# Kernel tuning notes

Hardware: AMD Instinct MI355X
Metric: run time of the kernel (lower is better)

## Reference

```python
import jax, jax.numpy as jnp
import numpy as np

L, V, Tctx, D, H, DFF = 4, 32000, 1024, 1024, 16, 4096
HD = D // H
B, T = 2, 1024


def _ln(x, w, b):
    mu = jnp.mean(x, axis=-1, keepdims=True)
    var = jnp.var(x, axis=-1, keepdims=True)
    return (x - mu) * jax.lax.rsqrt(var + 1e-5) * w + b


def setup_inputs() -> dict:
    key = jax.random.key(0)
    ks = jax.random.split(key, 8)
    s = 0.02
    return {
        "idx": jax.random.randint(ks[0], (B, T), 0, V),
        "wte": jax.random.normal(ks[1], (V, D), jnp.float32) * s,
        "wpe": jax.random.normal(ks[2], (Tctx, D), jnp.float32) * s,
        "ln1_w": jnp.ones((L, D), jnp.float32),
        "ln1_b": jnp.zeros((L, D), jnp.float32),
        "qkv_w": jax.random.normal(ks[3], (L, 3 * D, D), jnp.float32) * s,
        "qkv_b": jnp.zeros((L, 3 * D), jnp.float32),
        "proj_w": jax.random.normal(ks[4], (L, D, D), jnp.float32) * s,
        "proj_b": jnp.zeros((L, D), jnp.float32),
        "ln2_w": jnp.ones((L, D), jnp.float32),
        "ln2_b": jnp.zeros((L, D), jnp.float32),
        "fc1_w": jax.random.normal(ks[5], (L, DFF, D), jnp.float32) * s,
        "fc1_b": jnp.zeros((L, DFF), jnp.float32),
        "fc2_w": jax.random.normal(ks[6], (L, D, DFF), jnp.float32) * s,
        "fc2_b": jnp.zeros((L, D), jnp.float32),
        "lnf_w": jnp.ones((D,), jnp.float32),
        "lnf_b": jnp.zeros((D,), jnp.float32),
    }


def reference(idx, wte, wpe, ln1_w, ln1_b, qkv_w, qkv_b, proj_w, proj_b,
              ln2_w, ln2_b, fc1_w, fc1_b, fc2_w, fc2_b, lnf_w, lnf_b):
    b, t = idx.shape
    x = wte[idx] + wpe[:t]  # (B,T,D); dropout=0 (eval)
    scale = 1.0 / jnp.sqrt(jnp.float32(HD))
    causal = jnp.tril(jnp.ones((t, t), bool))  # (T,T)

    def block(x, p):
        (l1w, l1b, qw, qb, pw, pb, l2w, l2b, f1w, f1b, f2w, f2b) = p
        h = _ln(x, l1w, l1b)
        qkv = h @ qw.T + qb  # (B,T,3D)
        q, k, v = jnp.split(qkv, 3, axis=-1)
        q = q.reshape(b, t, H, HD)
        k = k.reshape(b, t, H, HD)
        v = v.reshape(b, t, H, HD)
        att = jnp.einsum('bqhd,bkhd->bhqk', q, k) * scale
        att = jnp.where(causal, att, -jnp.inf)
        att = jax.nn.softmax(att, axis=-1)
        y = jnp.einsum('bhqk,bkhd->bqhd', att, v).reshape(b, t, D)
        x = x + y @ pw.T + pb
        h2 = _ln(x, l2w, l2b)
        h2 = jax.nn.gelu(h2 @ f1w.T + f1b, approximate=False)
        x = x + h2 @ f2w.T + f2b
        return x, None

    params = (ln1_w, ln1_b, qkv_w, qkv_b, proj_w, proj_b,
              ln2_w, ln2_b, fc1_w, fc1_b, fc2_w, fc2_b)
    x, _ = jax.lax.scan(block, x, params)
    x = _ln(x, lnf_w, lnf_b)
    logits = x @ wte.T  # weight-tied lm_head
    return logits
```

## Files before the change

### kernel.cpp

```cpp
#include <hip/hip_runtime.h>
#include <hip/hip_bf16.h>
#include <cstdint>
#include <cstddef>

using hb = __hip_bfloat16;
typedef __bf16 bf16x8 __attribute__((ext_vector_type(8)));
typedef float f32x4 __attribute__((ext_vector_type(4)));
typedef const __attribute__((address_space(1))) void* gptr_t;
typedef __attribute__((address_space(3))) void* lptr_t;

namespace {
constexpr int L_ = 4, V_ = 32000, D_ = 1024, H_ = 16, DFF_ = 4096, HD_ = 64;
constexpr int B_ = 2, T_ = 1024;
constexpr int BT = B_ * T_;
constexpr int PSTR = 56;
constexpr int MTILES = BT / 128;
}

__global__ __launch_bounds__(256) void k_cast_bf16(const float* __restrict__ in,
                                                   hb* __restrict__ out, int n4) {
  int i = blockIdx.x * 256 + threadIdx.x;
  const int stride = gridDim.x * 256;
  for (; i < n4; i += stride) {
    float4 v = reinterpret_cast<const float4*>(in)[i];
    union { hb h[4]; ushort4 u; } t;
    t.h[0] = __float2bfloat16(v.x);
    t.h[1] = __float2bfloat16(v.y);
    t.h[2] = __float2bfloat16(v.z);
    t.h[3] = __float2bfloat16(v.w);
    reinterpret_cast<ushort4*>(out)[i] = t.u;
  }
}

__global__ __launch_bounds__(256) void k_embed(const int* __restrict__ idx,
                                               const float* __restrict__ wte,
                                               const float* __restrict__ wpe,
                                               float* __restrict__ x) {
  const int i = blockIdx.x * 256 + threadIdx.x;
  const int row = i >> 10;
  const int d = i & 1023;
  const int t = row & (T_ - 1);
  const int tok = idx[row];
  x[i] = wte[(size_t)tok * D_ + d] + wpe[(size_t)t * D_ + d];
}

__global__ __launch_bounds__(256) void k_ln(const float* __restrict__ x,
                                            const float* __restrict__ w,
                                            const float* __restrict__ b,
                                            hb* __restrict__ out) {
  const int row = blockIdx.x;
  const int tid = threadIdx.x;
  const float4 v = reinterpret_cast<const float4*>(x + (size_t)row * D_)[tid];
  float s = v.x + v.y + v.z + v.w;
  float ss = v.x * v.x + v.y * v.y + v.z * v.z + v.w * v.w;
#pragma unroll
  for (int o = 32; o; o >>= 1) { s += __shfl_xor(s, o); ss += __shfl_xor(ss, o); }
  __shared__ float rs[4], rss[4];
  const int wid = tid >> 6;
  if ((tid & 63) == 0) { rs[wid] = s; rss[wid] = ss; }
  __syncthreads();
  s = rs[0] + rs[1] + rs[2] + rs[3];
  ss = rss[0] + rss[1] + rss[2] + rss[3];
  const float mu = s * (1.f / D_);
  const float var = ss * (1.f / D_) - mu * mu;
  const float rstd = rsqrtf(var + 1e-5f);
  const float4 wv = reinterpret_cast<const float4*>(w)[tid];
  const float4 bv = reinterpret_cast<const float4*>(b)[tid];
  union { hb h[4]; ushort4 u; } t;
  t.h[0] = __float2bfloat16((v.x - mu) * rstd * wv.x + bv.x);
  t.h[1] = __float2bfloat16((v.y - mu) * rstd * wv.y + bv.y);
  t.h[2] = __float2bfloat16((v.z - mu) * rstd * wv.z + bv.z);
  t.h[3] = __float2bfloat16((v.w - mu) * rstd * wv.w + bv.w);
  reinterpret_cast<ushort4*>(out + (size_t)row * D_)[tid] = t.u;
}

__global__ __launch_bounds__(256) void k_vtrans(const hb* __restrict__ qkv,
                                                hb* __restrict__ vt) {
  __shared__ __align__(16) hb tile[64][66];
  const int bh = blockIdx.x;
  const int b = bh >> 4, h = bh & (H_ - 1);
  const int t0 = blockIdx.y * 64;
  const int tid = threadIdx.x;
  const int tl = tid >> 2, dc = (tid & 3) * 16;
  const hb* src = qkv + ((size_t)(b * T_ + t0 + tl) * 3 * D_) + 2 * D_ + h * HD_ + dc;
  *reinterpret_cast<bf16x8*>(&tile[tl][dc]) = *reinterpret_cast<const bf16x8*>(src);
  *reinterpret_cast<bf16x8*>(&tile[tl][dc + 8]) = *reinterpret_cast<const bf16x8*>(src + 8);
  __syncthreads();
  const int d = tid & 63, tj = tid >> 6;
  hb o[16];
#pragma unroll
  for (int j = 0; j < 16; ++j) o[j] = tile[tj * 16 + j][d];
  bf16x8* dst = reinterpret_cast<bf16x8*>(vt + ((size_t)bh * HD_ + d) * T_ + t0 + tj * 16);
  dst[0] = *reinterpret_cast<bf16x8*>(&o[0]);
  dst[1] = *reinterpret_cast<bf16x8*>(&o[8]);
}

__global__ __launch_bounds__(256) void k_attn(const hb* __restrict__ qkv,
                                              const hb* __restrict__ vt,
                                              hb* __restrict__ y) {
  const int lane = threadIdx.x & 63;
  const int wid = threadIdx.x >> 6;
  const int gw = blockIdx.x * 4 + wid;
  const int qt = 63 - (gw & 63);
  const int bh = gw >> 6;
  const int h = bh & (H_ - 1), b = bh >> 4;
  const int q0 = qt * 16;
  const int lr = lane & 15, g = lane >> 4;

  __shared__ __align__(16) hb plds[4][16 * PSTR];
  hb* pw = plds[wid];

  const size_t qrow = ((size_t)(b * T_ + q0 + lr) * 3 * D_) + (size_t)h * HD_;
  const bf16x8 qa0 = *reinterpret_cast<const bf16x8*>(qkv + qrow + g * 8);
  const bf16x8 qa1 = *reinterpret_cast<const bf16x8*>(qkv + qrow + 32 + g * 8);

  const f32x4 z = {0.f, 0.f, 0.f, 0.f};
  float m[4] = {-1e30f, -1e30f, -1e30f, -1e30f};
  float lsum[4] = {0.f, 0.f, 0.f, 0.f};
  f32x4 o[4];
#pragma unroll
  for (int i = 0; i < 4; ++i) o[i] = z;

  const int nkv = (q0 + 47) >> 5;
  for (int kt = 0; kt < nkv; ++kt) {
    const int kv0 = kt * 32;
    f32x4 s[2];
#pragma unroll
    for (int nt = 0; nt < 2; ++nt) {
      const size_t krow =
          ((size_t)(b * T_ + kv0 + nt * 16 + lr) * 3 * D_) + D_ + (size_t)h * HD_;
      const bf16x8 kb0 = *reinterpret_cast<const bf16x8*>(qkv + krow + g * 8);
      const bf16x8 kb1 = *reinterpret_cast<const bf16x8*>(qkv + krow + 32 + g * 8);
      f32x4 acc = z;
      acc = __builtin_amdgcn_mfma_f32_16x16x32_bf16(qa0, kb0, acc, 0, 0, 0);
      acc = __builtin_amdgcn_mfma_f32_16x16x32_bf16(qa1, kb1, acc, 0, 0, 0);
      s[nt] = acc;
    }
#pragma unroll
    for (int r = 0; r < 4; ++r) {
      const int qg = q0 + g * 4 + r;
      const float s0 = (kv0 + lr <= qg) ? s[0][r] * 0.125f : -1e30f;
      const float s1 = (kv0 + 16 + lr <= qg) ? s[1][r] * 0.125f : -1e30f;
      float rmax = fmaxf(s0, s1);
#pragma unroll
      for (int off = 1; off < 16; off <<= 1) rmax = fmaxf(rmax, __shfl_xor(rmax, off));
      const float mn = fmaxf(m[r], rmax);
      const float c = __expf(m[r] - mn);
      m[r] = mn;
      const float p0 = __expf(s0 - mn);
      const float p1 = __expf(s1 - mn);
      float ps = p0 + p1;
#pragma unroll
      for (int off = 1; off < 16; off <<= 1) ps += __shfl_xor(ps, off);
      lsum[r] = lsum[r] * c + ps;
#pragma unroll
      for (int dt = 0; dt < 4; ++dt) o[dt][r] *= c;
      pw[(g * 4 + r) * PSTR + lr] = __float2bfloat16(p0);
      pw[(g * 4 + r) * PSTR + 16 + lr] = __float2bfloat16(p1);
    }
    const bf16x8 pa = *reinterpret_cast<const bf16x8*>(&pw[lr * PSTR + g * 8]);
#pragma unroll
    for (int dt = 0; dt < 4; ++dt) {
      const bf16x8 vb = *reinterpret_cast<const bf16x8*>(
          vt + ((size_t)bh * HD_ + dt * 16 + lr) * T_ + kv0 + g * 8);
      o[dt] = __builtin_amdgcn_mfma_f32_16x16x32_bf16(pa, vb, o[dt], 0, 0, 0);
    }
  }
#pragma unroll
  for (int dt = 0; dt < 4; ++dt) {
#pragma unroll
    for (int r = 0; r < 4; ++r) {
      const size_t oo =
          ((size_t)(b * T_ + q0 + g * 4 + r) * D_) + h * HD_ + dt * 16 + lr;
      y[oo] = __float2bfloat16(o[dt][r] / lsum[r]);
    }
  }
}

template <int EPI, bool OBF, int BN>
__global__ __launch_bounds__(256) void gemm_bt(const hb* __restrict__ A,
                                               const hb* __restrict__ Bw,
                                               const float* __restrict__ bias,
                                               const float* resid,
                                               void* outv, int M, int N, int K) {
  constexpr int WMR = (BN == 128) ? 4 : 2;
  __shared__ __align__(16) hb As[2][128 * 32];
  __shared__ __align__(16) hb Bs[2][BN * 32];
  const int tid = threadIdx.x, lane = tid & 63, wid = tid >> 6;

  const int nwg = gridDim.x;
  const int d = blockIdx.x;
  const int wg = (d & 7) * (nwg >> 3) + (d >> 3);
  const int m0 = (wg & (MTILES - 1)) * 128;
  const int n0 = (wg / MTILES) * BN;

  const int wr = (BN == 128) ? (wid >> 1) : wid;
  const int wc = (BN == 128) ? (wid & 1) : 0;

  f32x4 acc[WMR][4];
  const f32x4 z = {0.f, 0.f, 0.f, 0.f};
#pragma unroll
  for (int i = 0; i < WMR; ++i)
#pragma unroll
    for (int j = 0; j < 4; ++j) acc[i][j] = z;

  const int e0 = tid * 8;
  auto stage = [&](int buf, int k0) {
#pragma unroll
    for (int r = 0; r < 2; ++r) {
      const int e = e0 + r * 2048;
      const int row = e >> 5, col = e & 31;
      __builtin_amdgcn_global_load_lds(
          (gptr_t)(A + (size_t)(m0 + row) * K + k0 + col), (lptr_t)(&As[buf][e]), 16, 0, 0);
    }
#pragma unroll
    for (int r = 0; r < BN / 64; ++r) {
      const int e = e0 + r * 2048;
      const int row = e >> 5, col = e & 31;
      __builtin_amdgcn_global_load_lds(
          (gptr_t)(Bw + (size_t)(n0 + row) * K + k0 + col), (lptr_t)(&Bs[buf][e]), 16, 0, 0);
    }
  };

  stage(0, 0);
  stage(1, 32);

  const int nt = K >> 5;
  const int lr = lane & 15, lk = (lane >> 4) * 8;
  for (int t = 0; t < nt; ++t) {
    const int cur = t & 1;
    if (t + 1 < nt) {
      if constexpr (BN == 128)
        asm volatile("s_waitcnt vmcnt(4)" ::: "memory");
      else
        asm volatile("s_waitcnt vmcnt(3)" ::: "memory");
    } else {
      asm volatile("s_waitcnt vmcnt(0)" ::: "memory");
    }
    asm volatile("s_barrier" ::: "memory");

    bf16x8 af[WMR], bfr[4];
#pragma unroll
    for (int i = 0; i < WMR; ++i)
      af[i] = *reinterpret_cast<const bf16x8*>(
          &As[cur][(wr * (WMR * 16) + i * 16 + lr) * 32 + lk]);
#pragma unroll
    for (int j = 0; j < 4; ++j)
      bfr[j] = *reinterpret_cast<const bf16x8*>(
          &Bs[cur][(wc * 64 + j * 16 + lr) * 32 + lk]);
#pragma unroll
    for (int i = 0; i < WMR; ++i)
#pragma unroll
      for (int j = 0; j < 4; ++j)
        acc[i][j] = __builtin_amdgcn_mfma_f32_16x16x32_bf16(af[i], bfr[j], acc[i][j], 0, 0, 0);

    asm volatile("s_waitcnt lgkmcnt(0)" ::: "memory");
    asm volatile("s_barrier" ::: "memory");
    if (t + 2 < nt) stage(cur, (t + 2) * 32);
  }

  const int lc = lane & 15, lr4 = (lane >> 4) * 4;
#pragma unroll
  for (int i = 0; i < WMR; ++i) {
    const int grow0 = m0 + wr * (WMR * 16) + i * 16 + lr4;
#pragma unroll
    for (int j = 0; j < 4; ++j) {
      const int gcol = n0 + wc * 64 + j * 16 + lc;
      const float bv = bias ? bias[gcol] : 0.f;
#pragma unroll
      for (int r = 0; r < 4; ++r) {
        const size_t oo = (size_t)(grow0 + r) * N + gcol;
        float val = acc[i][j][r] + bv;
        if constexpr (EPI == 1) val += resid[oo];
        if constexpr (EPI == 2) val = 0.5f * val * (1.f + erff(val * 0.70710678118f));
        if constexpr (OBF)
          reinterpret_cast<hb*>(outv)[oo] = __float2bfloat16(val);
        else
          reinterpret_cast<float*>(outv)[oo] = val;
      }
    }
  }
}

#define MM16(ABASE, AF, BF)                                                     \
  _Pragma("unroll") for (int i_ = 0; i_ < 4; ++i_)                              \
      _Pragma("unroll") for (int j_ = 0; j_ < 4; ++j_)                          \
          acc[(ABASE) + i_][j_] = __builtin_amdgcn_mfma_f32_16x16x32_bf16(      \
              (AF)[i_], (BF)[j_], acc[(ABASE) + i_][j_], 0, 0, 0);

__global__ __launch_bounds__(512, 2) void gemm_lmhead(const hb* __restrict__ A,
                                                      const hb* __restrict__ Bw,
                                                      float* __restrict__ out) {
  constexpr int K = 1024, N = 32000, NT = K / 32;
  __shared__ __align__(16) hb As[4][256][32];
  __shared__ __align__(16) hb Bs[4][256][32];
  const int tid = threadIdx.x, lane = tid & 63, wid = tid >> 6;
  const int nwg = gridDim.x;
  const int dd = blockIdx.x;
  const int wg = (dd & 7) * (nwg >> 3) + (dd >> 3);
  const int m0 = (wg & 7) * 256;
  const int n0 = (wg >> 3) * 256;
  const int wr = wid >> 2, wc = wid & 3;
  const int lr = lane & 15;
  const int rc8 = (((lane >> 4) ^ ((lr >> 1) & 3)) & 3) * 8;

  f32x4 acc[8][4];
  const f32x4 z = {0.f, 0.f, 0.f, 0.f};
#pragma unroll
  for (int i = 0; i < 8; ++i)
#pragma unroll
    for (int j = 0; j < 4; ++j) acc[i][j] = z;

  const int rr = tid >> 2;
  const int cs = tid & 3;
  const int cc = cs ^ ((tid >> 3) & 3);

  auto stageA = [&](int b, int t) {
#pragma unroll
    for (int q = 0; q < 2; ++q) {
      const int row = q * 128 + rr;
      __builtin_amdgcn_global_load_lds(
          (gptr_t)(A + (size_t)(m0 + row) * K + t * 32 + cc * 8),
          (lptr_t)(&As[b][row][cs * 8]), 16, 0, 0);
    }
  };
  auto stageB = [&](int b, int t) {
#pragma unroll
    for (int q = 0; q < 2; ++q) {
      const int row = q * 128 + rr;
      __builtin_amdgcn_global_load_lds(
          (gptr_t)(Bw + (size_t)(n0 + row) * K + t * 32 + cc * 8),
          (lptr_t)(&Bs[b][row][cs * 8]), 16, 0, 0);
    }
  };
  auto dsA = [&](int b, int mh, bf16x8* af) {
#pragma unroll
    for (int i = 0; i < 4; ++i)
      af[i] = *reinterpret_cast<const bf16x8*>(
          &As[b][wr * 128 + mh * 64 + i * 16 + lr][rc8]);
  };
  auto dsB = [&](int b, bf16x8* bf) {
#pragma unroll
    for (int j = 0; j < 4; ++j)
      bf[j] = *reinterpret_cast<const bf16x8*>(&Bs[b][wc * 64 + j * 16 + lr][rc8]);
  };

  auto tile = [&](int t, bool stg, int vm) {
    const int c = t & 3;
    const int b3 = (t + 3) & 3;
    bf16x8 af[4], bf[4];
    dsA(c, 0, af);
    dsB(c, bf);
    if (stg) stageA(b3, t + 3);
    __builtin_amdgcn_s_barrier();
    asm volatile("s_waitcnt lgkmcnt(0)" ::: "memory");
    __builtin_amdgcn_s_setprio(1);
    MM16(0, af, bf)
    __builtin_amdgcn_s_setprio(0);
    __builtin_amdgcn_s_barrier();
    dsA(c, 1, af);
    if (stg) stageB(b3, t + 3);
    if (vm == 8)
      asm volatile("s_waitcnt vmcnt(8)" ::: "memory");
    else if (vm == 4)
      asm volatile("s_waitcnt vmcnt(4)" ::: "memory");
    else if (vm == 0)
      asm volatile("s_waitcnt vmcnt(0)" ::: "memory");
    __builtin_amdgcn_s_barrier();
    asm volatile("s_waitcnt lgkmcnt(0)" ::: "memory");
    __builtin_amdgcn_s_setprio(1);
    MM16(4, af, bf)
    __builtin_amdgcn_s_setprio(0);
    __builtin_amdgcn_s_barrier();
  };

  stageA(0, 0); stageB(0, 0);
  stageA(1, 1); stageB(1, 1);
  stageA(2, 2); stageB(2, 2);
  asm volatile("s_waitcnt vmcnt(8)" ::: "memory");
  __builtin_amdgcn_s_barrier();

  for (int t = 0; t < NT - 3; ++t) tile(t, true, 8);
  tile(NT - 3, false, 4);
  tile(NT - 2, false, 0);
  tile(NT - 1, false, -1);

  const int lc = lane & 15, lr4 = (lane >> 4) * 4;
#pragma unroll
  for (int i2 = 0; i2 < 8; ++i2) {
    const int grow0 = m0 + wr * 128 + i2 * 16 + lr4;
#pragma unroll
    for (int j = 0; j < 4; ++j) {
      const int gcol = n0 + wc * 64 + j * 16 + lc;
#pragma unroll
      for (int r = 0; r < 4; ++r)
        out[(size_t)(grow0 + r) * N + gcol] = acc[i2][j][r];
    }
  }
}

extern "C" void kernel_launch(void* const* d_in, const int* in_sizes, int n_in,
                              void* d_out, int out_size, void* d_ws, size_t ws_size,
                              hipStream_t stream) {
  const int* idx = (const int*)d_in[0];
  const float* wte = (const float*)d_in[1];
  const float* wpe = (const float*)d_in[2];
  const float* ln1_w = (const float*)d_in[3];
  const float* ln1_b = (const float*)d_in[4];
  const float* qkv_w = (const float*)d_in[5];
  const float* qkv_b = (const float*)d_in[6];
  const float* proj_w = (const float*)d_in[7];
  const float* proj_b = (const float*)d_in[8];
  const float* ln2_w = (const float*)d_in[9];
  const float* ln2_b = (const float*)d_in[10];
  const float* fc1_w = (const float*)d_in[11];
  const float* fc1_b = (const float*)d_in[12];
  const float* fc2_w = (const float*)d_in[13];
  const float* fc2_b = (const float*)d_in[14];
  const float* lnf_w = (const float*)d_in[15];
  const float* lnf_b = (const float*)d_in[16];

  char* ws = (char*)d_ws;
  size_t off = 0;
  auto alloc = [&](size_t bytes) -> void* {
    void* p = ws + off;
    off += (bytes + 255) & ~(size_t)255;
    return p;
  };
  hb* wte_bf = (hb*)alloc((size_t)V_ * D_ * 2);
  hb* qkvw_bf = (hb*)alloc((size_t)L_ * 3 * D_ * D_ * 2);
  hb* projw_bf = (hb*)alloc((size_t)L_ * D_ * D_ * 2);
  hb* fc1w_bf = (hb*)alloc((size_t)L_ * DFF_ * D_ * 2);
  hb* fc2w_bf = (hb*)alloc((size_t)L_ * D_ * DFF_ * 2);
  float* x = (float*)alloc((size_t)BT * D_ * 4);
  hb* hbuf = (hb*)alloc((size_t)BT * D_ * 2);
  hb* qkvbuf = (hb*)alloc((size_t)BT * 3 * D_ * 2);
  hb* ybuf = (hb*)alloc((size_t)BT * D_ * 2);
  hb* gbuf = (hb*)alloc((size_t)BT * DFF_ * 2);
  hb* vtbuf = (hb*)alloc((size_t)B_ * H_ * HD_ * T_ * 2);

  auto cast = [&](const float* src, hb* dst, size_t n) {
    int n4 = (int)(n / 4);
    int blocks = (n4 + 255) / 256;
    if (blocks > 4096) blocks = 4096;
    k_cast_bf16<<<blocks, 256, 0, stream>>>(src, dst, n4);
  };
  cast(wte, wte_bf, (size_t)V_ * D_);
  cast(qkv_w, qkvw_bf, (size_t)L_ * 3 * D_ * D_);
  cast(proj_w, projw_bf, (size_t)L_ * D_ * D_);
  cast(fc1_w, fc1w_bf, (size_t)L_ * DFF_ * D_);
  cast(fc2_w, fc2w_bf, (size_t)L_ * D_ * DFF_);

  k_embed<<<BT * D_ / 256, 256, 0, stream>>>(idx, wte, wpe, x);

  for (int l = 0; l < L_; ++l) {
    k_ln<<<BT, 256, 0, stream>>>(x, ln1_w + l * D_, ln1_b + l * D_, hbuf);
    gemm_bt<0, true, 128><<<MTILES * (3 * D_ / 128), 256, 0, stream>>>(
        hbuf, qkvw_bf + (size_t)l * 3 * D_ * D_, qkv_b + (size_t)l * 3 * D_, nullptr,
        qkvbuf, BT, 3 * D_, D_);
    k_vtrans<<<dim3(B_ * H_, T_ / 64), 256, 0, stream>>>(qkvbuf, vtbuf);
    k_attn<<<(B_ * H_ * (T_ / 16)) / 4, 256, 0, stream>>>(qkvbuf, vtbuf, ybuf);
    gemm_bt<1, false, 64><<<MTILES * (D_ / 64), 256, 0, stream>>>(
        ybuf, projw_bf + (size_t)l * D_ * D_, proj_b + (size_t)l * D_, x, x, BT, D_, D_);
    k_ln<<<BT, 256, 0, stream>>>(x, ln2_w + l * D_, ln2_b + l * D_, hbuf);
    gemm_bt<2, true, 128><<<MTILES * (DFF_ / 128), 256, 0, stream>>>(
        hbuf, fc1w_bf + (size_t)l * DFF_ * D_, fc1_b + (size_t)l * DFF_, nullptr,
        gbuf, BT, DFF_, D_);
    gemm_bt<1, false, 64><<<MTILES * (D_ / 64), 256, 0, stream>>>(
        gbuf, fc2w_bf + (size_t)l * D_ * DFF_, fc2_b + (size_t)l * D_, x, x, BT, D_, DFF_);
  }

  k_ln<<<BT, 256, 0, stream>>>(x, lnf_w, lnf_b, hbuf);
  gemm_lmhead<<<8 * (V_ / 256), 512, 0, stream>>>(hbuf, wte_bf, (float*)d_out);
}
```

Before: 1.214 ms.

## Fuse V-transpose into QKV GEMM epilogue, merge casts and embed+LN

The QKV GEMM epilogue now also writes the V part straight into the transposed per-head layout, so the separate transpose kernel is gone. The five weight-cast launches become one multi-range kernel. Embedding is fused with the first layer's LayerNorm, which saves one launch and one pass over x. The cost is extra scattered 8-byte stores in the QKV epilogue.

```diff
diff --git a/kernel.cpp b/kernel.cpp
--- a/kernel.cpp
+++ b/kernel.cpp
@@ -17,11 +17,10 @@
 constexpr int MTILES = BT / 128;
 }
 
-__global__ __launch_bounds__(256) void k_cast_bf16(const float* __restrict__ in,
-                                                   hb* __restrict__ out, int n4) {
-  int i = blockIdx.x * 256 + threadIdx.x;
-  const int stride = gridDim.x * 256;
-  for (; i < n4; i += stride) {
+__device__ __forceinline__ void cast_range(const float* __restrict__ in,
+                                           hb* __restrict__ out, int n4,
+                                           int base, int stride) {
+  for (int i = base; i < n4; i += stride) {
     float4 v = reinterpret_cast<const float4*>(in)[i];
     union { hb h[4]; ushort4 u; } t;
     t.h[0] = __float2bfloat16(v.x);
@@ -32,16 +31,55 @@
   }
 }
 
-__global__ __launch_bounds__(256) void k_embed(const int* __restrict__ idx,
-                                               const float* __restrict__ wte,
-                                               const float* __restrict__ wpe,
-                                               float* __restrict__ x) {
-  const int i = blockIdx.x * 256 + threadIdx.x;
-  const int row = i >> 10;
-  const int d = i & 1023;
+__global__ __launch_bounds__(256) void k_cast5(
+    const float* s0, hb* d0, int n0, const float* s1, hb* d1, int n1,
+    const float* s2, hb* d2, int n2, const float* s3, hb* d3, int n3,
+    const float* s4, hb* d4, int n4) {
+  const int base = blockIdx.x * 256 + threadIdx.x;
+  const int stride = gridDim.x * 256;
+  cast_range(s0, d0, n0, base, stride);
+  cast_range(s1, d1, n1, base, stride);
+  cast_range(s2, d2, n2, base, stride);
+  cast_range(s3, d3, n3, base, stride);
+  cast_range(s4, d4, n4, base, stride);
+}
+
+__global__ __launch_bounds__(256) void k_embed_ln(const int* __restrict__ idx,
+                                                  const float* __restrict__ wte,
+                                                  const float* __restrict__ wpe,
+                                                  const float* __restrict__ w,
+                                                  const float* __restrict__ b,
+                                                  float* __restrict__ x,
+                                                  hb* __restrict__ out) {
+  const int row = blockIdx.x;
+  const int tid = threadIdx.x;
   const int t = row & (T_ - 1);
   const int tok = idx[row];
-  x[i] = wte[(size_t)tok * D_ + d] + wpe[(size_t)t * D_ + d];
+  const float4 a = reinterpret_cast<const float4*>(wte + (size_t)tok * D_)[tid];
+  const float4 p = reinterpret_cast<const float4*>(wpe + (size_t)t * D_)[tid];
+  const float4 v = {a.x + p.x, a.y + p.y, a.z + p.z, a.w + p.w};
+  reinterpret_cast<float4*>(x + (size_t)row * D_)[tid] = v;
+  float s = v.x + v.y + v.z + v.w;
+  float ss = v.x * v.x + v.y * v.y + v.z * v.z + v.w * v.w;
+#pragma unroll
+  for (int o = 32; o; o >>= 1) { s += __shfl_xor(s, o); ss += __shfl_xor(ss, o); }
+  __shared__ float rs[4], rss[4];
+  const int wid = tid >> 6;
+  if ((tid & 63) == 0) { rs[wid] = s; rss[wid] = ss; }
+  __syncthreads();
+  s = rs[0] + rs[1] + rs[2] + rs[3];
+  ss = rss[0] + rss[1] + rss[2] + rss[3];
+  const float mu = s * (1.f / D_);
+  const float var = ss * (1.f / D_) - mu * mu;
+  const float rstd = rsqrtf(var + 1e-5f);
+  const float4 wv = reinterpret_cast<const float4*>(w)[tid];
+  const float4 bv = reinterpret_cast<const float4*>(b)[tid];
+  union { hb h[4]; ushort4 u; } o2;
+  o2.h[0] = __float2bfloat16((v.x - mu) * rstd * wv.x + bv.x);
+  o2.h[1] = __float2bfloat16((v.y - mu) * rstd * wv.y + bv.y);
+  o2.h[2] = __float2bfloat16((v.z - mu) * rstd * wv.z + bv.z);
+  o2.h[3] = __float2bfloat16((v.w - mu) * rstd * wv.w + bv.w);
+  reinterpret_cast<ushort4*>(out + (size_t)row * D_)[tid] = o2.u;
 }
 
 __global__ __launch_bounds__(256) void k_ln(const float* __restrict__ x,
@@ -74,27 +112,6 @@
   reinterpret_cast<ushort4*>(out + (size_t)row * D_)[tid] = t.u;
 }
 
-__global__ __launch_bounds__(256) void k_vtrans(const hb* __restrict__ qkv,
-                                                hb* __restrict__ vt) {
-  __shared__ __align__(16) hb tile[64][66];
-  const int bh = blockIdx.x;
-  const int b = bh >> 4, h = bh & (H_ - 1);
-  const int t0 = blockIdx.y * 64;
-  const int tid = threadIdx.x;
-  const int tl = tid >> 2, dc = (tid & 3) * 16;
-  const hb* src = qkv + ((size_t)(b * T_ + t0 + tl) * 3 * D_) + 2 * D_ + h * HD_ + dc;
-  *reinterpret_cast<bf16x8*>(&tile[tl][dc]) = *reinterpret_cast<const bf16x8*>(src);
-  *reinterpret_cast<bf16x8*>(&tile[tl][dc + 8]) = *reinterpret_cast<const bf16x8*>(src + 8);
-  __syncthreads();
-  const int d = tid & 63, tj = tid >> 6;
-  hb o[16];
-#pragma unroll
-  for (int j = 0; j < 16; ++j) o[j] = tile[tj * 16 + j][d];
-  bf16x8* dst = reinterpret_cast<bf16x8*>(vt + ((size_t)bh * HD_ + d) * T_ + t0 + tj * 16);
-  dst[0] = *reinterpret_cast<bf16x8*>(&o[0]);
-  dst[1] = *reinterpret_cast<bf16x8*>(&o[8]);
-}
-
 __global__ __launch_bounds__(256) void k_attn(const hb* __restrict__ qkv,
                                               const hb* __restrict__ vt,
                                               hb* __restrict__ y) {
@@ -177,12 +194,13 @@
   }
 }
 
-template <int EPI, bool OBF, int BN>
+template <int EPI, bool OBF, int BN, bool WVT>
 __global__ __launch_bounds__(256) void gemm_bt(const hb* __restrict__ A,
                                                const hb* __restrict__ Bw,
                                                const float* __restrict__ bias,
                                                const float* resid,
-                                               void* outv, int M, int N, int K) {
+                                               void* outv, hb* __restrict__ vt,
+                                               int M, int N, int K) {
   constexpr int WMR = (BN == 128) ? 4 : 2;
   __shared__ __align__(16) hb As[2][128 * 32];
   __shared__ __align__(16) hb Bs[2][BN * 32];
@@ -267,16 +285,30 @@
     for (int j = 0; j < 4; ++j) {
       const int gcol = n0 + wc * 64 + j * 16 + lc;
       const float bv = bias ? bias[gcol] : 0.f;
+      union { hb h[4]; ushort4 u; } vv;
 #pragma unroll
       for (int r = 0; r < 4; ++r) {
         const size_t oo = (size_t)(grow0 + r) * N + gcol;
         float val = acc[i][j][r] + bv;
         if constexpr (EPI == 1) val += resid[oo];
         if constexpr (EPI == 2) val = 0.5f * val * (1.f + erff(val * 0.70710678118f));
-        if constexpr (OBF)
-          reinterpret_cast<hb*>(outv)[oo] = __float2bfloat16(val);
-        else
+        if constexpr (OBF) {
+          const hb hv = __float2bfloat16(val);
+          reinterpret_cast<hb*>(outv)[oo] = hv;
+          if constexpr (WVT) vv.h[r] = hv;
+        } else {
           reinterpret_cast<float*>(outv)[oo] = val;
+        }
+      }
+      if constexpr (WVT) {
+        if (gcol >= 2 * D_) {
+          const int vcol = gcol - 2 * D_;
+          const int b = grow0 >> 10;
+          const int t0 = grow0 & (T_ - 1);
+          *reinterpret_cast<ushort4*>(
+              vt + ((size_t)(b * H_ + (vcol >> 6)) * HD_ + (vcol & 63)) * T_ + t0) =
+              vv.u;
+        }
       }
     }
   }
@@ -439,35 +471,31 @@
   hb* gbuf = (hb*)alloc((size_t)BT * DFF_ * 2);
   hb* vtbuf = (hb*)alloc((size_t)B_ * H_ * HD_ * T_ * 2);
 
-  auto cast = [&](const float* src, hb* dst, size_t n) {
-    int n4 = (int)(n / 4);
-    int blocks = (n4 + 255) / 256;
-    if (blocks > 4096) blocks = 4096;
-    k_cast_bf16<<<blocks, 256, 0, stream>>>(src, dst, n4);
-  };
-  cast(wte, wte_bf, (size_t)V_ * D_);
-  cast(qkv_w, qkvw_bf, (size_t)L_ * 3 * D_ * D_);
-  cast(proj_w, projw_bf, (size_t)L_ * D_ * D_);
-  cast(fc1_w, fc1w_bf, (size_t)L_ * DFF_ * D_);
-  cast(fc2_w, fc2w_bf, (size_t)L_ * D_ * DFF_);
-
-  k_embed<<<BT * D_ / 256, 256, 0, stream>>>(idx, wte, wpe, x);
+  k_cast5<<<4096, 256, 0, stream>>>(
+      wte, wte_bf, (int)((size_t)V_ * D_ / 4),
+      qkv_w, qkvw_bf, (int)((size_t)L_ * 3 * D_ * D_ / 4),
+      proj_w, projw_bf, (int)((size_t)L_ * D_ * D_ / 4),
+      fc1_w, fc1w_bf, (int)((size_t)L_ * DFF_ * D_ / 4),
+      fc2_w, fc2w_bf, (int)((size_t)L_ * D_ * DFF_ / 4));
+
+  k_embed_ln<<<BT, 256, 0, stream>>>(idx, wte, wpe, ln1_w, ln1_b, x, hbuf);
 
   for (int l = 0; l < L_; ++l) {
-    k_ln<<<BT, 256, 0, stream>>>(x, ln1_w + l * D_, ln1_b + l * D_, hbuf);
-    gemm_bt<0, true, 128><<<MTILES * (3 * D_ / 128), 256, 0, stream>>>(
+    if (l) k_ln<<<BT, 256, 0, stream>>>(x, ln1_w + l * D_, ln1_b + l * D_, hbuf);
+    gemm_bt<0, true, 128, true><<<MTILES * (3 * D_ / 128), 256, 0, stream>>>(
         hbuf, qkvw_bf + (size_t)l * 3 * D_ * D_, qkv_b + (size_t)l * 3 * D_, nullptr,
-        qkvbuf, BT, 3 * D_, D_);
-    k_vtrans<<<dim3(B_ * H_, T_ / 64), 256, 0, stream>>>(qkvbuf, vtbuf);
+        qkvbuf, vtbuf, BT, 3 * D_, D_);
     k_attn<<<(B_ * H_ * (T_ / 16)) / 4, 256, 0, stream>>>(qkvbuf, vtbuf, ybuf);
-    gemm_bt<1, false, 64><<<MTILES * (D_ / 64), 256, 0, stream>>>(
-        ybuf, projw_bf + (size_t)l * D_ * D_, proj_b + (size_t)l * D_, x, x, BT, D_, D_);
+    gemm_bt<1, false, 64, false><<<MTILES * (D_ / 64), 256, 0, stream>>>(
+        ybuf, projw_bf + (size_t)l * D_ * D_, proj_b + (size_t)l * D_, x, x, nullptr,
+        BT, D_, D_);
     k_ln<<<BT, 256, 0, stream>>>(x, ln2_w + l * D_, ln2_b + l * D_, hbuf);
-    gemm_bt<2, true, 128><<<MTILES * (DFF_ / 128), 256, 0, stream>>>(
+    gemm_bt<2, true, 128, false><<<MTILES * (DFF_ / 128), 256, 0, stream>>>(
         hbuf, fc1w_bf + (size_t)l * DFF_ * D_, fc1_b + (size_t)l * DFF_, nullptr,
-        gbuf, BT, DFF_, D_);
-    gemm_bt<1, false, 64><<<MTILES * (D_ / 64), 256, 0, stream>>>(
-        gbuf, fc2w_bf + (size_t)l * D_ * DFF_, fc2_b + (size_t)l * D_, x, x, BT, D_, DFF_);
+        gbuf, nullptr, BT, DFF_, D_);
+    gemm_bt<1, false, 64, false><<<MTILES * (D_ / 64), 256, 0, stream>>>(
+        gbuf, fc2w_bf + (size_t)l * D_ * DFF_, fc2_b + (size_t)l * D_, x, x, nullptr,
+        BT, D_, DFF_);
   }
 
   k_ln<<<BT, 256, 0, stream>>>(x, lnf_w, lnf_b, hbuf);
```

Measured after the change: 1.268 ms. 1.04x slower.
